# Optimization experiments

Hardware: AMD Instinct MI355X
Metric: run time of the kernel (lower is better)

Reference implementation:

```python
import jax, jax.numpy as jnp
import numpy as np

B, R, T, F_IN, L, D, H, OUT, ES = 8, 128, 64, 32, 64, 64, 128, 32, 2048
DT = 0.1  # dt_step from init


def _glorot(key, shape):
    scale = 1.0 / np.sqrt(shape[0])
    return (jax.random.normal(key, shape, jnp.float32) * scale).astype(jnp.float32)


def setup_inputs() -> dict:
    key = jax.random.key(0)
    ks = jax.random.split(key, 20)
    return {
        "node_feats": jax.random.normal(ks[0], (B, R, T, F_IN), jnp.float32),
        "eps": jax.random.normal(ks[1], (B, R, L + D), jnp.float32),
        "space_w": jax.random.uniform(ks[2], (B, ES), jnp.float32),
        "src": jax.random.randint(ks[3], (ES,), 0, R, jnp.int32),
        "dst": jax.random.randint(ks[4], (ES,), 0, R, jnp.int32),
        "W_e1": _glorot(ks[5], (F_IN + 1, H)),
        "b_e1": jnp.zeros((H,), jnp.float32),
        "W_e2": _glorot(ks[6], (H, H)),
        "b_e2": jnp.zeros((H,), jnp.float32),
        "W_mu": _glorot(ks[7], (H, L + D)),
        "W_sig": _glorot(ks[8], (H, L + D)),
        "W_msg": _glorot(ks[9], (L, L)),
        "W_self": _glorot(ks[10], (L, L)),
        "W_dyn": _glorot(ks[11], (D, L)),
        "b_ode": jnp.zeros((L,), jnp.float32),
        "W_d1": _glorot(ks[12], (L + D + 1 + R, H)),
        "b_d1": jnp.zeros((H,), jnp.float32),
        "W_d2": _glorot(ks[13], (H, OUT)),
        "b_d2": jnp.zeros((OUT,), jnp.float32),
    }


def reference(node_feats, eps, space_w, src, dst,
              W_e1, b_e1, W_e2, b_e2, W_mu, W_sig,
              W_msg, W_self, W_dyn, b_ode,
              W_d1, b_d1, W_d2, b_d2):
    dt = jnp.asarray(DT, node_feats.dtype)
    tgrid = jnp.arange(T, dtype=node_feats.dtype) / T  # normalized time, like t/t.max()
    t_feat = jnp.broadcast_to(tgrid[None, None, :, None], (B, R, T, 1))

    # ---- Encoder: node features + time -> per-node mu/sigma (NP-style) ----
    x = jnp.concatenate([node_feats, t_feat], axis=-1)          # [B,R,T,F+1]
    h = jax.nn.silu(x @ W_e1 + b_e1)
    h = jax.nn.silu(h @ W_e2 + b_e2)
    hp = h.mean(axis=2)                                          # pool over time -> [B,R,H]
    mu = hp @ W_mu                                               # [B,R,L+D]
    sigma = 0.1 + 0.9 * jax.nn.sigmoid(hp @ W_sig)
    v = mu + sigma * eps                                         # reparameterized latent
    Lz, Dz = v[..., :L], v[..., L:]                              # integrated state / h_dyn

    # ---- MPGCN ODE func: weighted edge gather/scatter + self + h_dyn ----
    dyn = Dz @ W_dyn                                             # constant conditioning [B,R,L]

    def f(xs):                                                   # xs: [B,R,L]
        m = space_w[..., None] * xs[:, src, :]                   # per-edge message [B,E,L]
        agg = jnp.zeros((B, R, L), xs.dtype).at[:, dst].add(m)   # sum aggregation
        return jnp.tanh(agg @ W_msg + xs @ W_self + dyn + b_ode)

    # ---- RK4 fixed-step integrator, save state at every time point ----
    def step(xs, _):
        k1 = f(xs)
        k2 = f(xs + 0.5 * dt * k1)
        k3 = f(xs + 0.5 * dt * k2)
        k4 = f(xs + dt * k3)
        xn = xs + (dt / 6.0) * (k1 + 2.0 * k2 + 2.0 * k3 + k4)
        return xn, xn

    _, traj = jax.lax.scan(step, Lz, None, length=T)             # [T,B,R,L]
    traj = jnp.moveaxis(traj, 0, 2)                              # [B,R,T,L]

    # ---- Decoder: [L(t), h_dyn, time, region one-hot] -> y ----
    rid = jnp.broadcast_to(jnp.eye(R, dtype=traj.dtype)[None, :, None, :], (B, R, T, R))
    d_rep = jnp.broadcast_to(Dz[:, :, None, :], (B, R, T, D))
    dec_in = jnp.concatenate([traj, d_rep, t_feat, rid], axis=-1)  # [B,R,T,257]
    hd = jax.nn.silu(dec_in @ W_d1 + b_d1)
    y = hd @ W_d2 + b_d2                                         # [B,R,T,OUT]
    return y
```

## Files before the change

### kernel.cpp

```cpp
#include <hip/hip_runtime.h>

#define B_ 8
#define R_ 128
#define T_ 64
#define FIN_ 32
#define L_ 64
#define D_ 64
#define H_ 128
#define OUT_ 32
#define ES_ 2048

typedef _Float16 f16;
typedef __attribute__((ext_vector_type(2))) _Float16 f16x2;
typedef __attribute__((ext_vector_type(4))) _Float16 f16x4;
typedef __attribute__((ext_vector_type(8))) _Float16 f16x8;
typedef __attribute__((ext_vector_type(16))) float f32x16;

__device__ __forceinline__ float silu_f(float x) { return x / (1.f + __expf(-x)); }
__device__ __forceinline__ float tanh_f(float x) {
    float e = __expf(2.f * x);
    return 1.f - 2.f / (e + 1.f);
}

__device__ __forceinline__ uint32_t swzP(uint32_t r, uint32_t cByte) {
    return (r * 256u + cByte) ^ ((r & 15u) << 4);
}
__device__ __forceinline__ uint32_t swzT(uint32_t c, uint32_t s, uint32_t rByte) {
    uint32_t bo = c * 512u + s * 256u + rByte;
    return bo ^ ((c & 31u) << 4);
}

#define XP_OFF 0u
#define MT_OFF 32768u
#define ODE_LDS 65536u

__global__ __launch_bounds__(128) void prep_kernel(
    const int* __restrict__ src, const int* __restrict__ dst,
    const float* __restrict__ space_w,
    int* __restrict__ row_start, int* __restrict__ esrcp, float* __restrict__ wperm) {
    __shared__ int cnt[R_];
    __shared__ int rs[R_ + 1];
    __shared__ int permS[ES_];
    int r = threadIdx.x;
    int c = 0;
    for (int e = 0; e < ES_; ++e) c += (dst[e] == r) ? 1 : 0;
    cnt[r] = c;
    __syncthreads();
    if (r == 0) {
        int a = 0;
        for (int i = 0; i < R_; ++i) { rs[i] = a; a += cnt[i]; }
        rs[R_] = a;
    }
    __syncthreads();
    {
        int k = rs[r];
        for (int e = 0; e < ES_; ++e)
            if (dst[e] == r) permS[k++] = e;
    }
    __syncthreads();
    row_start[r] = rs[r];
    if (r == 0) row_start[R_] = rs[R_];
    for (int e = r; e < ES_; e += 128) esrcp[e] = src[permS[e]];
    for (int i = r; i < B_ * ES_; i += 128) {
        int b = i >> 11;
        int e = i & (ES_ - 1);
        wperm[i] = space_w[b * ES_ + permS[e]];
    }
}

__global__ __launch_bounds__(256) void encoder_kernel(
    const float* __restrict__ node_feats, const float* __restrict__ eps,
    const float* __restrict__ W_e1, const float* __restrict__ b_e1,
    const float* __restrict__ W_e2, const float* __restrict__ b_e2,
    const float* __restrict__ W_mu, const float* __restrict__ W_sig,
    const float* __restrict__ W_dyn,
    float* __restrict__ Lz, float* __restrict__ Dz, float* __restrict__ dynb) {
    int br = blockIdx.x;
    int tid = threadIdx.x;
    __shared__ __align__(16) float xS[T_ * 36];
    __shared__ __align__(16) float h1[T_ * H_];
    __shared__ float hps[2 * H_];
    __shared__ float hp[H_];
    __shared__ float muS[H_], sgS[H_], vS[H_];

    const float* nf = node_feats + (size_t)br * (T_ * FIN_);
    for (int i = tid; i < T_ * FIN_; i += 256) {
        int t = i >> 5, f = i & 31;
        xS[t * 36 + f] = nf[i];
    }
    if (tid < T_) xS[tid * 36 + 32] = (float)tid * (1.f / 64.f);

    int j = tid & 127;
    int th = tid >> 7;
    float we1r[33];
    #pragma unroll
    for (int k = 0; k < 33; ++k) we1r[k] = W_e1[k * H_ + j];
    __syncthreads();

    float be1 = b_e1[j];
    for (int tt = 0; tt < 32; ++tt) {
        int t = th * 32 + tt;
        float a = be1;
        const float4* xr = (const float4*)(&xS[t * 36]);
        #pragma unroll
        for (int w4 = 0; w4 < 8; ++w4) {
            float4 xv = xr[w4];
            a += xv.x * we1r[w4 * 4 + 0] + xv.y * we1r[w4 * 4 + 1] +
                 xv.z * we1r[w4 * 4 + 2] + xv.w * we1r[w4 * 4 + 3];
        }
        a += xS[t * 36 + 32] * we1r[32];
        h1[t * H_ + j] = silu_f(a);
    }
    __syncthreads();

    float acc[32];
    float be2 = b_e2[j];
    #pragma unroll
    for (int tt = 0; tt < 32; ++tt) acc[tt] = be2;
    for (int kc = 0; kc < 4; ++kc) {
        float wreg[32];
        #pragma unroll
        for (int i2 = 0; i2 < 32; ++i2) wreg[i2] = W_e2[(kc * 32 + i2) * H_ + j];
        #pragma unroll
        for (int tt = 0; tt < 32; ++tt) {
            int t = th * 32 + tt;
            const float4* hrow = (const float4*)(&h1[t * H_ + kc * 32]);
            float s = 0.f;
            #pragma unroll
            for (int w4 = 0; w4 < 8; ++w4) {
                float4 hv = hrow[w4];
                s += hv.x * wreg[w4 * 4 + 0] + hv.y * wreg[w4 * 4 + 1] +
                     hv.z * wreg[w4 * 4 + 2] + hv.w * wreg[w4 * 4 + 3];
            }
            acc[tt] += s;
        }
    }
    float msum = 0.f;
    #pragma unroll
    for (int tt = 0; tt < 32; ++tt) msum += silu_f(acc[tt]);
    hps[th * H_ + j] = msum;
    __syncthreads();
    if (tid < H_) hp[tid] = (hps[tid] + hps[H_ + tid]) * (1.f / 64.f);
    __syncthreads();

    {
        const float* Wm = (th == 0) ? W_mu : W_sig;
        float a = 0.f;
        #pragma unroll 4
        for (int k = 0; k < H_; ++k) a += hp[k] * Wm[k * H_ + j];
        if (th == 0) muS[j] = a; else sgS[j] = a;
    }
    __syncthreads();
    if (tid < H_) {
        float sig = 0.1f + 0.9f / (1.f + __expf(-sgS[tid]));
        float v = muS[tid] + sig * eps[(size_t)br * H_ + tid];
        vS[tid] = v;
        if (tid < L_) Lz[(size_t)br * L_ + tid] = v;
        else          Dz[(size_t)br * D_ + (tid - L_)] = v;
    }
    __syncthreads();
    if (tid < L_) {
        float a = 0.f;
        #pragma unroll 4
        for (int k = 0; k < D_; ++k) a += vS[L_ + k] * W_dyn[k * L_ + tid];
        dynb[(size_t)br * L_ + tid] = a;
    }
}

__global__ __launch_bounds__(512, 2) void ode_kernel(
    const float* __restrict__ Lz, const float* __restrict__ dynb,
    const float* __restrict__ W_msg, const float* __restrict__ W_self,
    const float* __restrict__ b_ode,
    const int* __restrict__ row_start, const int* __restrict__ esrcp,
    const float* __restrict__ wperm,
    float* __restrict__ traj) {
    const int b = blockIdx.x;
    const int tid = threadIdx.x;
    const int lane = tid & 63;
    const int w = tid >> 6;
    const int rb = w & 3;
    const int cb = w >> 2;
    const int l31 = lane & 31;
    const int h = lane >> 5;
    const int cc = cb * 32 + l31;

    extern __shared__ char sm[];
    float* Af = (float*)sm;

    f16x8 wsH[4], wsL[4], wmH[4], wmL[4];
    #pragma unroll
    for (int m = 0; m < 4; ++m) {
        f16x8 sh, sl, mh, ml;
        #pragma unroll
        for (int i = 0; i < 8; ++i) {
            int k = m * 16 + 8 * h + i;
            float vs = W_self[k * 64 + cc];
            f16 s0 = (f16)vs;
            sh[i] = s0; sl[i] = (f16)(vs - (float)s0);
            float vm = W_msg[k * 64 + cc];
            f16 m0 = (f16)vm;
            mh[i] = m0; ml[i] = (f16)(vm - (float)m0);
        }
        wsH[m] = sh; wsL[m] = sl; wmH[m] = mh; wmL[m] = ml;
    }

    for (int i = tid; i < 128 * 128; i += 512) Af[i] = 0.f;
    __syncthreads();
    if (tid < 128) {
        int e0 = row_start[tid], e1 = row_start[tid + 1];
        for (int e = e0; e < e1; ++e)
            Af[tid * 128 + esrcp[e]] += wperm[b * ES_ + e];
    }
    __syncthreads();

    f16x8 aH[8], aL[8];
    {
        int row = rb * 32 + l31;
        #pragma unroll
        for (int m = 0; m < 8; ++m) {
            const float* p = Af + row * 128 + m * 16 + h * 8;
            f16x8 vh, vl;
            #pragma unroll
            for (int i = 0; i < 8; ++i) {
                float v = p[i];
                f16 hi = (f16)v;
                vh[i] = hi;
                vl[i] = (f16)(v - (float)hi);
            }
            aH[m] = vh;
            aL[m] = vl;
        }
    }

    float xb[16], ks[16], dnb[16];
    {
        float bo = b_ode[cc];
        #pragma unroll
        for (int i = 0; i < 16; ++i) {
            int r = rb * 32 + (i & 3) + 8 * (i >> 2) + 4 * h;
            size_t o = ((size_t)(b * R_ + r)) * L_ + cc;
            xb[i] = Lz[o];
            dnb[i] = dynb[o] + bo;
        }
    }
    __syncthreads();

    #pragma unroll
    for (int i = 0; i < 16; ++i) {
        int r = rb * 32 + (i & 3) + 8 * (i >> 2) + 4 * h;
        f16 hi = (f16)xb[i];
        f16x2 pk; pk[0] = hi; pk[1] = (f16)(xb[i] - (float)hi);
        *(f16x2*)(sm + XP_OFF + swzP(r, cc * 4)) = pk;
    }
    __syncthreads();

    const int rowx = rb * 32 + l31;

    for (int n = 0; n < T_; ++n) {
        #pragma unroll
        for (int i = 0; i < 16; ++i) ks[i] = 0.f;
        for (int s4 = 0; s4 < 4; ++s4) {
            const float wk = (s4 == 1 || s4 == 2) ? 2.f : 1.f;
            const float cn = (s4 < 2) ? 0.05f : 0.1f;

            f32x16 accS, accM = {};
            #pragma unroll
            for (int i = 0; i < 16; ++i) accS[i] = dnb[i];
            #pragma unroll
            for (int m = 0; m < 4; ++m) {
                uint32_t cByte = (m * 16 + 8 * h) * 4;
                uint4 p0 = *(const uint4*)(sm + XP_OFF + swzP(rowx, cByte));
                uint4 p1 = *(const uint4*)(sm + XP_OFF + swzP(rowx, cByte + 16));
                union { uint32_t u[4]; f16x8 v; } axh, axl;
                axh.u[0] = (p0.x & 0xFFFFu) | (p0.y << 16);
                axh.u[1] = (p0.z & 0xFFFFu) | (p0.w << 16);
                axh.u[2] = (p1.x & 0xFFFFu) | (p1.y << 16);
                axh.u[3] = (p1.z & 0xFFFFu) | (p1.w << 16);
                axl.u[0] = (p0.x >> 16) | (p0.y & 0xFFFF0000u);
                axl.u[1] = (p0.z >> 16) | (p0.w & 0xFFFF0000u);
                axl.u[2] = (p1.x >> 16) | (p1.y & 0xFFFF0000u);
                axl.u[3] = (p1.z >> 16) | (p1.w & 0xFFFF0000u);
                accS = __builtin_amdgcn_mfma_f32_32x32x16_f16(axh.v, wsH[m], accS, 0, 0, 0);
                accM = __builtin_amdgcn_mfma_f32_32x32x16_f16(axh.v, wmH[m], accM, 0, 0, 0);
                accS = __builtin_amdgcn_mfma_f32_32x32x16_f16(axl.v, wsH[m], accS, 0, 0, 0);
                accM = __builtin_amdgcn_mfma_f32_32x32x16_f16(axl.v, wmH[m], accM, 0, 0, 0);
                accS = __builtin_amdgcn_mfma_f32_32x32x16_f16(axh.v, wsL[m], accS, 0, 0, 0);
                accM = __builtin_amdgcn_mfma_f32_32x32x16_f16(axh.v, wmL[m], accM, 0, 0, 0);
            }
            #pragma unroll
            for (int q = 0; q < 4; ++q) {
                int rbase = rb * 32 + 8 * q + 4 * h;
                f16x4 vh, vl;
                #pragma unroll
                for (int u = 0; u < 4; ++u) {
                    float t = accM[4 * q + u];
                    f16 hi = (f16)t;
                    vh[u] = hi;
                    vl[u] = (f16)(t - (float)hi);
                }
                *(f16x4*)(sm + MT_OFF + swzT(cc, 0, rbase * 2)) = vh;
                *(f16x4*)(sm + MT_OFF + swzT(cc, 1, rbase * 2)) = vl;
            }
            __syncthreads();

            f32x16 accP = {}, accQ = {};
            #pragma unroll
            for (int m = 0; m < 8; ++m) {
                f16x8 mtH = *(const f16x8*)(sm + MT_OFF + swzT(cc, 0, (m * 16 + 8 * h) * 2));
                f16x8 mtL = *(const f16x8*)(sm + MT_OFF + swzT(cc, 1, (m * 16 + 8 * h) * 2));
                if (m & 1) {
                    accQ = __builtin_amdgcn_mfma_f32_32x32x16_f16(aH[m], mtH, accQ, 0, 0, 0);
                    accQ = __builtin_amdgcn_mfma_f32_32x32x16_f16(aL[m], mtH, accQ, 0, 0, 0);
                    accQ = __builtin_amdgcn_mfma_f32_32x32x16_f16(aH[m], mtL, accQ, 0, 0, 0);
                } else {
                    accP = __builtin_amdgcn_mfma_f32_32x32x16_f16(aH[m], mtH, accP, 0, 0, 0);
                    accP = __builtin_amdgcn_mfma_f32_32x32x16_f16(aL[m], mtH, accP, 0, 0, 0);
                    accP = __builtin_amdgcn_mfma_f32_32x32x16_f16(aH[m], mtL, accP, 0, 0, 0);
                }
            }
            float xn_[16];
            #pragma unroll
            for (int i = 0; i < 16; ++i) {
                float kv = tanh_f(accS[i] + accP[i] + accQ[i]);
                ks[i] += wk * kv;
                xn_[i] = (s4 < 3) ? (xb[i] + cn * kv) : (xb[i] + (0.1f / 6.f) * ks[i]);
            }
            if (s4 == 3) {
                #pragma unroll
                for (int i = 0; i < 16; ++i) xb[i] = xn_[i];
            }
            #pragma unroll
            for (int i = 0; i < 16; ++i) {
                int r = rb * 32 + (i & 3) + 8 * (i >> 2) + 4 * h;
                f16 hi = (f16)xn_[i];
                f16x2 pk; pk[0] = hi; pk[1] = (f16)(xn_[i] - (float)hi);
                *(f16x2*)(sm + XP_OFF + swzP(r, cc * 4)) = pk;
            }
            if (s4 == 3) {
                #pragma unroll
                for (int i = 0; i < 16; ++i) {
                    int r = rb * 32 + (i & 3) + 8 * (i >> 2) + 4 * h;
                    traj[(((size_t)b * T_ + n) * R_ + r) * L_ + cc] = xb[i];
                }
            }
            __syncthreads();
        }
    }
}

__global__ __launch_bounds__(256) void decoder_kernel(
    const float* __restrict__ traj, const float* __restrict__ Dz,
    const float* __restrict__ W_d1, const float* __restrict__ b_d1,
    const float* __restrict__ W_d2, const float* __restrict__ b_d2,
    float* __restrict__ y) {
    int br = blockIdx.x;
    int b = br >> 7;
    int r = br & 127;
    int tid = threadIdx.x;
    __shared__ __align__(16) float trajS[32 * L_];
    __shared__ __align__(16) float hS[32 * H_];
    __shared__ float dzS[D_];
    __shared__ float baseS[H_];

    int j = tid & 127;
    int th = tid >> 7;
    if (tid < D_) dzS[tid] = Dz[(size_t)br * D_ + tid];
    __syncthreads();

    float wcol[64];
    #pragma unroll
    for (int k = 0; k < 64; ++k) wcol[k] = W_d1[k * H_ + j];
    float wt = W_d1[128 * H_ + j];
    if (th == 0) {
        float a = b_d1[j] + W_d1[(129 + r) * H_ + j];
        #pragma unroll 4
        for (int k = 0; k < D_; ++k) a += dzS[k] * W_d1[(64 + k) * H_ + j];
        baseS[j] = a;
    }
    __syncthreads();
    float bb = baseS[j];

    for (int half = 0; half < 2; ++half) {
        for (int i = tid; i < 32 * L_; i += 256) {
            int tt = i >> 6, l = i & 63;
            trajS[i] = traj[(((size_t)b * T_ + half * 32 + tt) * R_ + r) * L_ + l];
        }
        __syncthreads();
        #pragma unroll
        for (int tt = 0; tt < 16; ++tt) {
            int tl = th * 16 + tt;
            int t = half * 32 + tl;
            float a = bb + (float)t * (1.f / 64.f) * wt;
            const float4* tr4 = (const float4*)(&trajS[tl * L_]);
            #pragma unroll
            for (int kb = 0; kb < 16; ++kb) {
                float4 tv = tr4[kb];
                a += tv.x * wcol[kb * 4 + 0] + tv.y * wcol[kb * 4 + 1] +
                     tv.z * wcol[kb * 4 + 2] + tv.w * wcol[kb * 4 + 3];
            }
            hS[tl * H_ + j] = silu_f(a);
        }
        __syncthreads();
        {
            int o = tid & 31, q = tid >> 5;
            float acc2[4];
            float bd2 = b_d2[o];
            #pragma unroll
            for (int u = 0; u < 4; ++u) acc2[u] = bd2;
            for (int jc = 0; jc < 4; ++jc) {
                float wreg[32];
                #pragma unroll
                for (int i2 = 0; i2 < 32; ++i2) wreg[i2] = W_d2[(jc * 32 + i2) * OUT_ + o];
                #pragma unroll
                for (int u = 0; u < 4; ++u) {
                    int tl = q * 4 + u;
                    const float4* h4 = (const float4*)(&hS[tl * H_ + jc * 32]);
                    float s2 = 0.f;
                    #pragma unroll
                    for (int w4 = 0; w4 < 8; ++w4) {
                        float4 hv = h4[w4];
                        s2 += hv.x * wreg[w4 * 4 + 0] + hv.y * wreg[w4 * 4 + 1] +
                              hv.z * wreg[w4 * 4 + 2] + hv.w * wreg[w4 * 4 + 3];
                    }
                    acc2[u] += s2;
                }
            }
            #pragma unroll
            for (int u = 0; u < 4; ++u) {
                int t = half * 32 + q * 4 + u;
                y[((size_t)br * T_ + t) * OUT_ + o] = acc2[u];
            }
        }
        __syncthreads();
    }
}

extern "C" void kernel_launch(void* const* d_in, const int* in_sizes, int n_in,
                              void* d_out, int out_size, void* d_ws, size_t ws_size,
                              hipStream_t stream) {
    const float* node_feats = (const float*)d_in[0];
    const float* eps_       = (const float*)d_in[1];
    const float* space_w    = (const float*)d_in[2];
    const int*   src        = (const int*)d_in[3];
    const int*   dst        = (const int*)d_in[4];
    const float* W_e1 = (const float*)d_in[5];
    const float* b_e1 = (const float*)d_in[6];
    const float* W_e2 = (const float*)d_in[7];
    const float* b_e2 = (const float*)d_in[8];
    const float* W_mu = (const float*)d_in[9];
    const float* W_sig = (const float*)d_in[10];
    const float* W_msg = (const float*)d_in[11];
    const float* W_self = (const float*)d_in[12];
    const float* W_dyn = (const float*)d_in[13];
    const float* b_ode = (const float*)d_in[14];
    const float* W_d1 = (const float*)d_in[15];
    const float* b_d1 = (const float*)d_in[16];
    const float* W_d2 = (const float*)d_in[17];
    const float* b_d2 = (const float*)d_in[18];
    float* out = (float*)d_out;

    float* f_ws = (float*)d_ws;
    float* Lz    = f_ws;
    float* Dz    = Lz + B_ * R_ * L_;
    float* dynb  = Dz + B_ * R_ * D_;
    float* traj  = dynb + B_ * R_ * L_;
    float* wperm = traj + (size_t)B_ * T_ * R_ * L_;
    int* row_start = (int*)(wperm + B_ * ES_);
    int* esrcp     = row_start + 132;

    prep_kernel<<<1, 128, 0, stream>>>(src, dst, space_w, row_start, esrcp, wperm);
    encoder_kernel<<<B_ * R_, 256, 0, stream>>>(node_feats, eps_, W_e1, b_e1, W_e2, b_e2,
                                                W_mu, W_sig, W_dyn, Lz, Dz, dynb);
    ode_kernel<<<B_, 512, ODE_LDS, stream>>>(Lz, dynb, W_msg, W_self, b_ode,
                                             row_start, esrcp, wperm, traj);
    decoder_kernel<<<B_ * R_, 256, 0, stream>>>(traj, Dz, W_d1, b_d1, W_d2, b_d2, out);
}
```

Baseline: 1.761 ms.

## Move split-f16 ODE weights to LDS and split state into hi/lo planes

The W_self and W_msg hi/lo fp16 split fragments are now staged once into swizzled LDS and read inside each RK4 stage, where before they were held in registers. The x state is stored as separate hi and lo planes, so A-fragments load directly as f16x8 with no bit unpacking. The aggregation MFMA chain is spread over three accumulators instead of two to shorten dependency chains. This lowers VGPR pressure and ALU repacking, at the cost of extra LDS reads per stage and a larger LDS footprint (ODE_LDS grows to 96KB).

```diff
diff --git a/kernel.cpp b/kernel.cpp
--- a/kernel.cpp
+++ b/kernel.cpp
@@ -22,17 +22,20 @@
     return 1.f - 2.f / (e + 1.f);
 }
 
-__device__ __forceinline__ uint32_t swzP(uint32_t r, uint32_t cByte) {
-    return (r * 256u + cByte) ^ ((r & 15u) << 4);
+__device__ __forceinline__ uint32_t swz256(uint32_t row, uint32_t s, uint32_t colByte) {
+    uint32_t bo = row * 256u + s * 128u + colByte;
+    return bo ^ ((row & 15u) << 4);
 }
 __device__ __forceinline__ uint32_t swzT(uint32_t c, uint32_t s, uint32_t rByte) {
     uint32_t bo = c * 512u + s * 256u + rByte;
     return bo ^ ((c & 31u) << 4);
 }
 
-#define XP_OFF 0u
-#define MT_OFF 32768u
-#define ODE_LDS 65536u
+#define XROW_OFF 0u
+#define MT_OFF   32768u
+#define WS_OFF   65536u
+#define WM_OFF   81920u
+#define ODE_LDS  98304u
 
 __global__ __launch_bounds__(128) void prep_kernel(
     const int* __restrict__ src, const int* __restrict__ dst,
@@ -187,23 +190,17 @@
     extern __shared__ char sm[];
     float* Af = (float*)sm;
 
-    f16x8 wsH[4], wsL[4], wmH[4], wmL[4];
-    #pragma unroll
-    for (int m = 0; m < 4; ++m) {
-        f16x8 sh, sl, mh, ml;
-        #pragma unroll
-        for (int i = 0; i < 8; ++i) {
-            int k = m * 16 + 8 * h + i;
-            float vs = W_self[k * 64 + cc];
-            f16 s0 = (f16)vs;
-            sh[i] = s0; sl[i] = (f16)(vs - (float)s0);
-            float vm = W_msg[k * 64 + cc];
-            f16 m0 = (f16)vm;
-            mh[i] = m0; ml[i] = (f16)(vm - (float)m0);
-        }
-        wsH[m] = sh; wsL[m] = sl; wmH[m] = mh; wmL[m] = ml;
-    }
-
+    for (int idx = tid; idx < 4096; idx += 512) {
+        int j = idx & 63, k = idx >> 6;
+        float vs = W_self[k * 64 + j];
+        f16 sh = (f16)vs;
+        *(f16*)(sm + WS_OFF + swz256(j, 0, k * 2)) = sh;
+        *(f16*)(sm + WS_OFF + swz256(j, 1, k * 2)) = (f16)(vs - (float)sh);
+        float vm = W_msg[k * 64 + j];
+        f16 mh = (f16)vm;
+        *(f16*)(sm + WM_OFF + swz256(j, 0, k * 2)) = mh;
+        *(f16*)(sm + WM_OFF + swz256(j, 1, k * 2)) = (f16)(vm - (float)mh);
+    }
     for (int i = tid; i < 128 * 128; i += 512) Af[i] = 0.f;
     __syncthreads();
     if (tid < 128) {
@@ -249,8 +246,8 @@
     for (int i = 0; i < 16; ++i) {
         int r = rb * 32 + (i & 3) + 8 * (i >> 2) + 4 * h;
         f16 hi = (f16)xb[i];
-        f16x2 pk; pk[0] = hi; pk[1] = (f16)(xb[i] - (float)hi);
-        *(f16x2*)(sm + XP_OFF + swzP(r, cc * 4)) = pk;
+        *(f16*)(sm + XROW_OFF + swz256(r, 0, cc * 2)) = hi;
+        *(f16*)(sm + XROW_OFF + swz256(r, 1, cc * 2)) = (f16)(xb[i] - (float)hi);
     }
     __syncthreads();
 
@@ -263,29 +260,29 @@
             const float wk = (s4 == 1 || s4 == 2) ? 2.f : 1.f;
             const float cn = (s4 < 2) ? 0.05f : 0.1f;
 
-            f32x16 accS, accM = {};
-            #pragma unroll
-            for (int i = 0; i < 16; ++i) accS[i] = dnb[i];
+            f16x8 xh[4], xl[4];
             #pragma unroll
             for (int m = 0; m < 4; ++m) {
-                uint32_t cByte = (m * 16 + 8 * h) * 4;
-                uint4 p0 = *(const uint4*)(sm + XP_OFF + swzP(rowx, cByte));
-                uint4 p1 = *(const uint4*)(sm + XP_OFF + swzP(rowx, cByte + 16));
-                union { uint32_t u[4]; f16x8 v; } axh, axl;
-                axh.u[0] = (p0.x & 0xFFFFu) | (p0.y << 16);
-                axh.u[1] = (p0.z & 0xFFFFu) | (p0.w << 16);
-                axh.u[2] = (p1.x & 0xFFFFu) | (p1.y << 16);
-                axh.u[3] = (p1.z & 0xFFFFu) | (p1.w << 16);
-                axl.u[0] = (p0.x >> 16) | (p0.y & 0xFFFF0000u);
-                axl.u[1] = (p0.z >> 16) | (p0.w & 0xFFFF0000u);
-                axl.u[2] = (p1.x >> 16) | (p1.y & 0xFFFF0000u);
-                axl.u[3] = (p1.z >> 16) | (p1.w & 0xFFFF0000u);
-                accS = __builtin_amdgcn_mfma_f32_32x32x16_f16(axh.v, wsH[m], accS, 0, 0, 0);
-                accM = __builtin_amdgcn_mfma_f32_32x32x16_f16(axh.v, wmH[m], accM, 0, 0, 0);
-                accS = __builtin_amdgcn_mfma_f32_32x32x16_f16(axl.v, wsH[m], accS, 0, 0, 0);
-                accM = __builtin_amdgcn_mfma_f32_32x32x16_f16(axl.v, wmH[m], accM, 0, 0, 0);
-                accS = __builtin_amdgcn_mfma_f32_32x32x16_f16(axh.v, wsL[m], accS, 0, 0, 0);
-                accM = __builtin_amdgcn_mfma_f32_32x32x16_f16(axh.v, wmL[m], accM, 0, 0, 0);
+                uint32_t kB = (m * 16 + 8 * h) * 2;
+                xh[m] = *(const f16x8*)(sm + XROW_OFF + swz256(rowx, 0, kB));
+                xl[m] = *(const f16x8*)(sm + XROW_OFF + swz256(rowx, 1, kB));
+            }
+            f32x16 aS, aM = {};
+            #pragma unroll
+            for (int i = 0; i < 16; ++i) aS[i] = dnb[i];
+            #pragma unroll
+            for (int m = 0; m < 4; ++m) {
+                uint32_t kB = (m * 16 + 8 * h) * 2;
+                f16x8 wsH = *(const f16x8*)(sm + WS_OFF + swz256(cc, 0, kB));
+                f16x8 wsL = *(const f16x8*)(sm + WS_OFF + swz256(cc, 1, kB));
+                f16x8 wmH = *(const f16x8*)(sm + WM_OFF + swz256(cc, 0, kB));
+                f16x8 wmL = *(const f16x8*)(sm + WM_OFF + swz256(cc, 1, kB));
+                aS = __builtin_amdgcn_mfma_f32_32x32x16_f16(xh[m], wsH, aS, 0, 0, 0);
+                aM = __builtin_amdgcn_mfma_f32_32x32x16_f16(xh[m], wmH, aM, 0, 0, 0);
+                aS = __builtin_amdgcn_mfma_f32_32x32x16_f16(xl[m], wsH, aS, 0, 0, 0);
+                aM = __builtin_amdgcn_mfma_f32_32x32x16_f16(xl[m], wmH, aM, 0, 0, 0);
+                aS = __builtin_amdgcn_mfma_f32_32x32x16_f16(xh[m], wsL, aS, 0, 0, 0);
+                aM = __builtin_amdgcn_mfma_f32_32x32x16_f16(xh[m], wmL, aM, 0, 0, 0);
             }
             #pragma unroll
             for (int q = 0; q < 4; ++q) {
@@ -293,7 +290,7 @@
                 f16x4 vh, vl;
                 #pragma unroll
                 for (int u = 0; u < 4; ++u) {
-                    float t = accM[4 * q + u];
+                    float t = aM[4 * q + u];
                     f16 hi = (f16)t;
                     vh[u] = hi;
                     vl[u] = (f16)(t - (float)hi);
@@ -303,25 +300,29 @@
             }
             __syncthreads();
 
-            f32x16 accP = {}, accQ = {};
+            f32x16 e0 = {}, e1 = {}, e2 = {};
             #pragma unroll
             for (int m = 0; m < 8; ++m) {
                 f16x8 mtH = *(const f16x8*)(sm + MT_OFF + swzT(cc, 0, (m * 16 + 8 * h) * 2));
                 f16x8 mtL = *(const f16x8*)(sm + MT_OFF + swzT(cc, 1, (m * 16 + 8 * h) * 2));
-                if (m & 1) {
-                    accQ = __builtin_amdgcn_mfma_f32_32x32x16_f16(aH[m], mtH, accQ, 0, 0, 0);
-                    accQ = __builtin_amdgcn_mfma_f32_32x32x16_f16(aL[m], mtH, accQ, 0, 0, 0);
-                    accQ = __builtin_amdgcn_mfma_f32_32x32x16_f16(aH[m], mtL, accQ, 0, 0, 0);
+                if (m < 3) {
+                    e0 = __builtin_amdgcn_mfma_f32_32x32x16_f16(aH[m], mtH, e0, 0, 0, 0);
+                    e0 = __builtin_amdgcn_mfma_f32_32x32x16_f16(aL[m], mtH, e0, 0, 0, 0);
+                    e0 = __builtin_amdgcn_mfma_f32_32x32x16_f16(aH[m], mtL, e0, 0, 0, 0);
+                } else if (m < 6) {
+                    e1 = __builtin_amdgcn_mfma_f32_32x32x16_f16(aH[m], mtH, e1, 0, 0, 0);
+                    e1 = __builtin_amdgcn_mfma_f32_32x32x16_f16(aL[m], mtH, e1, 0, 0, 0);
+                    e1 = __builtin_amdgcn_mfma_f32_32x32x16_f16(aH[m], mtL, e1, 0, 0, 0);
                 } else {
-                    accP = __builtin_amdgcn_mfma_f32_32x32x16_f16(aH[m], mtH, accP, 0, 0, 0);
-                    accP = __builtin_amdgcn_mfma_f32_32x32x16_f16(aL[m], mtH, accP, 0, 0, 0);
-                    accP = __builtin_amdgcn_mfma_f32_32x32x16_f16(aH[m], mtL, accP, 0, 0, 0);
+                    e2 = __builtin_amdgcn_mfma_f32_32x32x16_f16(aH[m], mtH, e2, 0, 0, 0);
+                    e2 = __builtin_amdgcn_mfma_f32_32x32x16_f16(aL[m], mtH, e2, 0, 0, 0);
+                    e2 = __builtin_amdgcn_mfma_f32_32x32x16_f16(aH[m], mtL, e2, 0, 0, 0);
                 }
             }
             float xn_[16];
             #pragma unroll
             for (int i = 0; i < 16; ++i) {
-                float kv = tanh_f(accS[i] + accP[i] + accQ[i]);
+                float kv = tanh_f(aS[i] + e0[i] + e1[i] + e2[i]);
                 ks[i] += wk * kv;
                 xn_[i] = (s4 < 3) ? (xb[i] + cn * kv) : (xb[i] + (0.1f / 6.f) * ks[i]);
             }
@@ -333,8 +334,8 @@
             for (int i = 0; i < 16; ++i) {
                 int r = rb * 32 + (i & 3) + 8 * (i >> 2) + 4 * h;
                 f16 hi = (f16)xn_[i];
-                f16x2 pk; pk[0] = hi; pk[1] = (f16)(xn_[i] - (float)hi);
-                *(f16x2*)(sm + XP_OFF + swzP(r, cc * 4)) = pk;
+                *(f16*)(sm + XROW_OFF + swz256(r, 0, cc * 2)) = hi;
+                *(f16*)(sm + XROW_OFF + swz256(r, 1, cc * 2)) = (f16)(xn_[i] - (float)hi);
             }
             if (s4 == 3) {
                 #pragma unroll
```

After: 1.639 ms. -7.0%, faster.
